# Kernel optimization log

Measured on AMD Instinct MI355X. Metric: run time of the kernel, lower is better.

The kernel has to match this reference:

```python
import jax, jax.numpy as jnp
import numpy as np
from jax import lax

EPS = 1e-5  # BatchNorm eps; eval-mode BN with running_mean=0, running_var=1


def _bn(v, g, b):
    return v * (g / jnp.sqrt(1.0 + EPS)) + b


def setup_inputs() -> dict:
    key = jax.random.key(0)
    ks = jax.random.split(key, 8)
    B, I, O, H, W, E, K, r = 16, 128, 128, 128, 128, 16, 3, 8
    Ir, Or = I // r, O // r
    f = jax.random.normal
    return {
        "x": f(ks[0], (B, I, H, W), jnp.float32),
        "experts": f(ks[1], (E, O, I, K, K), jnp.float32) * 0.05,
        "rw1": f(ks[2], (Ir, I), jnp.float32) * 0.05,
        "rbn1_g": jnp.ones((Ir,), jnp.float32),
        "rbn1_b": jnp.zeros((Ir,), jnp.float32),
        "rw2": f(ks[3], (I, Ir), jnp.float32) * 0.05,
        "rbn2_g": jnp.ones((I,), jnp.float32),
        "rbn2_b": jnp.zeros((I,), jnp.float32),
        "rw3": f(ks[4], (E, I), jnp.float32) * 0.05,
        "rb3": jnp.zeros((E,), jnp.float32),
        "ca_w1": f(ks[5], (Or, O), jnp.float32) * 0.05,
        "ca_bn1_g": jnp.ones((Or,), jnp.float32),
        "ca_bn1_b": jnp.zeros((Or,), jnp.float32),
        "ca_w2": f(ks[6], (O, Or), jnp.float32) * 0.05,
        "ca_bn2_g": jnp.ones((O,), jnp.float32),
        "ca_bn2_b": jnp.zeros((O,), jnp.float32),
        "sa_w": f(ks[7], (1, 2, 7, 7), jnp.float32) * 0.05,
        "sa_bn_g": jnp.ones((1,), jnp.float32),
        "sa_bn_b": jnp.zeros((1,), jnp.float32),
    }


def reference(x, experts, rw1, rbn1_g, rbn1_b, rw2, rbn2_g, rbn2_b, rw3, rb3,
              ca_w1, ca_bn1_g, ca_bn1_b, ca_w2, ca_bn2_g, ca_bn2_b,
              sa_w, sa_bn_g, sa_bn_b):
    B, I, H, W = x.shape
    E, O, _, K, _ = experts.shape
    # --- routing: avgpool -> 1x1 conv (matmul) -> BN -> ReLU -> 1x1 -> BN -> sigmoid -> 1x1 -> softmax
    p = jnp.mean(x, axis=(2, 3))                                  # [B, I]
    h = jax.nn.relu(_bn(p @ rw1.T, rbn1_g, rbn1_b))               # [B, I/r]
    g = jax.nn.sigmoid(_bn(h @ rw2.T, rbn2_g, rbn2_b))            # [B, I]
    rweights = jax.nn.softmax(g @ rw3.T + rb3, axis=1)            # [B, E]
    # --- expert-weighted kernel generation as a single GEMM
    w = jnp.einsum('be,eoihw->boihw', rweights, experts)          # [B, O, I, K, K]
    # --- per-sample conv via grouped conv (groups = B), stride=1, padding=1
    out = lax.conv_general_dilated(
        x.reshape(1, B * I, H, W),
        w.reshape(B * O, I, K, K),
        window_strides=(1, 1), padding=((1, 1), (1, 1)),
        dimension_numbers=('NCHW', 'OIHW', 'NCHW'),
        feature_group_count=B,
    ).reshape(B, O, H, W)
    # --- SE channel attention
    cp = jnp.mean(out, axis=(2, 3))                               # [B, O]
    ch = jax.nn.relu(_bn(cp @ ca_w1.T, ca_bn1_g, ca_bn1_b))
    cw = jax.nn.sigmoid(_bn(ch @ ca_w2.T, ca_bn2_g, ca_bn2_b))    # [B, O]
    out = out * cw[:, :, None, None]
    # --- CBAM spatial attention
    sp = jnp.concatenate([jnp.mean(out, axis=1, keepdims=True),
                          jnp.max(out, axis=1, keepdims=True)], axis=1)  # [B,2,H,W]
    sw = lax.conv_general_dilated(sp, sa_w, (1, 1), ((3, 3), (3, 3)),
                                  dimension_numbers=('NCHW', 'OIHW', 'NCHW'))
    sw = jax.nn.sigmoid(_bn(sw, sa_bn_g.reshape(1, 1, 1, 1), sa_bn_b.reshape(1, 1, 1, 1)))
    out = out * sw
    # --- residual (in_channels == out_channels -> Identity)
    return out + x
```

## Files before the change

kernel.cpp:

```cpp
#include <hip/hip_runtime.h>

typedef unsigned short ushort_t;
typedef __attribute__((ext_vector_type(4))) float float4_t;
typedef __attribute__((ext_vector_type(8))) short short8_t;
typedef __attribute__((ext_vector_type(8))) unsigned short ushort8_t;
typedef __attribute__((ext_vector_type(4))) unsigned short ushort4_t;

__device__ __forceinline__ ushort_t f2bf(float f) {
    unsigned u = __builtin_bit_cast(unsigned, f);
    u = (u + 0x7fffu + ((u >> 16) & 1u)) >> 16;
    return (ushort_t)u;
}
__device__ __forceinline__ ushort_t f2h(float f) {
    return __builtin_bit_cast(unsigned short, (_Float16)f);
}
__device__ __forceinline__ float h2f(ushort_t u) {
    return (float)__builtin_bit_cast(_Float16, u);
}

__device__ __forceinline__ void gld16(const void* g, void* l) {
    __builtin_amdgcn_global_load_lds(
        (const __attribute__((address_space(1))) unsigned int*)g,
        (__attribute__((address_space(3))) unsigned int*)l, 16, 0, 0);
}


__global__ __launch_bounds__(256) void init_kernel(float* __restrict__ p,
                                                   float* __restrict__ sp,
                                                   ushort_t* __restrict__ xn,
                                                   float* __restrict__ st,
                                                   unsigned* __restrict__ wcnt,
                                                   const float* __restrict__ x) {
    int blk = blockIdx.x;
    int tid = threadIdx.x;
    if (blk >= 6381) {
        int bi = blk - 6381;
        const float* xb = x + (long)bi * 16384;
        int half = tid >> 7, t = tid & 127;
        __shared__ float red[2][2][128];
        __shared__ float corn[4];
        float rv = half ? xb[16256 + t] : xb[t];
        float cv = half ? xb[t * 128 + 127] : xb[t * 128];
        red[0][half][t] = rv;
        red[1][half][t] = cv;
        if (tid == 0)   corn[0] = rv;
        if (tid == 127) corn[1] = rv;
        if (tid == 128) corn[2] = rv;
        if (tid == 255) corn[3] = rv;
        __syncthreads();
        int wave = tid >> 6, lane = tid & 63;
        int kind = wave >> 1, hf = wave & 1;
        float s = red[kind][hf][lane] + red[kind][hf][lane + 64];
        for (int msk = 1; msk < 64; msk <<= 1) s += __shfl_xor(s, msk, 64);
        if (lane == 0) st[bi * 8 + kind * 2 + hf] = s;
        if (tid < 4) st[bi * 8 + 4 + tid] = corn[tid];
        return;
    }
    int t = blk * 256 + tid;
    if (t < 2048) { p[t] = 0.f; if (t == 0) *wcnt = 0u; return; }
    t -= 2048;
    if (t < 574592) { sp[t] = 0.f; return; }
    t -= 574592;
    if (t < 1056768) {
        int b = t / 66048;
        int r = t % 66048;
        int pix = r >> 7, i = r & 127;
        int hp, wp;
        if (pix < 130)      { hp = 0;   wp = pix; }
        else if (pix < 260) { hp = 129; wp = pix - 130; }
        else { int q = pix - 260; hp = 1 + (q >> 1); wp = (q & 1) ? 129 : 0; }
        xn[((b * 130 + hp) * 130 + wp) * 128 + i] = 0;
    }
}

__global__ __launch_bounds__(256) void transpose_kernel(const float* __restrict__ x,
                                                        ushort_t* __restrict__ xn,
                                                        float* __restrict__ p) {
    __shared__ float tile[128][65];
    int blk = blockIdx.x;
    int wt = blk & 1, h = (blk >> 1) & 127, b = blk >> 8;
    int w0 = wt * 64;
    int tid = threadIdx.x;
    int wl = tid & 63, ig = tid >> 6;
    const float* src = x + ((long)(b * 128) * 128 + h) * 128 + w0 + wl;
    #pragma unroll
    for (int i = ig; i < 128; i += 4) tile[i][wl] = src[(long)i * 16384];
    __syncthreads();
    if (tid < 128) {
        float s = 0.f;
        #pragma unroll
        for (int w = 0; w < 64; ++w) s += tile[tid][w];
        atomicAdd(&p[b * 128 + tid], s * (1.0f / 16384.0f));
    }
    int l16 = tid & 15, wq = tid >> 4;
    #pragma unroll
    for (int pass = 0; pass < 4; ++pass) {
        int w = wq + pass * 16;
        ushort8_t v;
        #pragma unroll
        for (int j = 0; j < 8; ++j) v[j] = f2bf(tile[l16 * 8 + j][w]);
        *(ushort8_t*)&xn[((b * 130 + h + 1) * 130 + (w0 + w + 1)) * 128 + l16 * 8] = v;
    }
}

__global__ __launch_bounds__(256) void wgen_kernel(const float* __restrict__ experts,
        const float* __restrict__ p, const float* __restrict__ st,
        const float* __restrict__ rw1, const float* __restrict__ g1, const float* __restrict__ b1,
        const float* __restrict__ rw2, const float* __restrict__ g2, const float* __restrict__ b2,
        const float* __restrict__ rw3, const float* __restrict__ rb3,
        const float* __restrict__ cw1, const float* __restrict__ cg1, const float* __restrict__ cb1,
        const float* __restrict__ cw2, const float* __restrict__ cg2, const float* __restrict__ cb2,
        ushort_t* __restrict__ w2, float* __restrict__ cp, float* __restrict__ cw,
        unsigned* __restrict__ wcnt) {
    int o = blockIdx.x;
    int tid = threadIdx.x;
    int lane = tid & 63, wave = tid >> 6;
    __shared__ __align__(16) float ex[16 * 1152];
    __shared__ float sg[16][128];
    __shared__ float sh[16][16];
    __shared__ float sl[16][16];
    __shared__ float rwl[16][16];
    __shared__ float cpw[4][8];
    __shared__ int lastf;

    const float* ebase = experts + (long)o * 1152;
    #pragma unroll
    for (int j = 0; j < 4; ++j) {
        int e = wave * 4 + j;
        const char* src = (const char*)(ebase + (long)e * 147456) + lane * 16;
        char* dst = (char*)&ex[e * 1152];
        #pragma unroll
        for (int k = 0; k < 5; ++k) {
            if (k < 4 || lane < 32)
                gld16(src + k * 1024, dst + k * 1024);
        }
    }

    const float bns = rsqrtf(1.0f + 1e-5f);
    {   int b = tid >> 4, j = tid & 15;
        float s = 0.f;
        for (int i = 0; i < 128; ++i) s += p[b * 128 + i] * rw1[j * 128 + i];
        s = s * (g1[j] * bns) + b1[j];
        sh[b][j] = fmaxf(s, 0.f); }
    __syncthreads();
    for (int c = 0; c < 8; ++c) {
        int idx = tid + c * 256;
        int b = idx >> 7, j = idx & 127;
        float s = 0.f;
        for (int k = 0; k < 16; ++k) s += sh[b][k] * rw2[j * 16 + k];
        s = s * (g2[j] * bns) + b2[j];
        sg[b][j] = 1.0f / (1.0f + expf(-s));
    }
    __syncthreads();
    {   int b = tid >> 4, e = tid & 15;
        float s = rb3[e];
        for (int j = 0; j < 128; ++j) s += sg[b][j] * rw3[e * 128 + j];
        sl[b][e] = s; }
    __syncthreads();
    {   int b = tid >> 4, e = tid & 15;
        float m = -1e30f;
        for (int k = 0; k < 16; ++k) m = fmaxf(m, sl[b][k]);
        float num = expf(sl[b][e] - m), den = 0.f;
        for (int k = 0; k < 16; ++k) den += expf(sl[b][k] - m);
        rwl[b][e] = num / den; }
    asm volatile("s_waitcnt vmcnt(0)" ::: "memory");
    __syncthreads();

    int i = tid & 127, half = tid >> 7;
    float acc[8][9];
    #pragma unroll
    for (int b = 0; b < 8; ++b)
        #pragma unroll
        for (int d = 0; d < 9; ++d) acc[b][d] = 0.f;
    for (int e = 0; e < 16; ++e) {
        float v[9];
        #pragma unroll
        for (int d = 0; d < 9; ++d) v[d] = ex[e * 1152 + i * 9 + d];
        #pragma unroll
        for (int b = 0; b < 8; ++b) {
            float r = rwl[half * 8 + b][e];
            #pragma unroll
            for (int d = 0; d < 9; ++d) acc[b][d] += v[d] * r;
        }
    }
    float cps[8];
    #pragma unroll
    for (int bb2 = 0; bb2 < 8; ++bb2) {
        int b = half * 8 + bb2;
        const float* sb = st + ((b << 7) + i) * 8;
        float T = p[(b << 7) + i] * 16384.f;
        float r0 = sb[0], r127 = sb[1], c0 = sb[2], c127 = sb[3];
        float x00 = sb[4], x0127 = sb[5], x1270 = sb[6], x127127 = sb[7];
        float S0 = T - r127 - c127 + x127127;
        float S1 = T - r127;
        float S2 = T - r127 - c0 + x1270;
        float S3 = T - c127;
        float S4 = T;
        float S5 = T - c0;
        float S6 = T - r0 - c127 + x0127;
        float S7 = T - r0;
        float S8 = T - r0 - c0 + x00;
        cps[bb2] = acc[bb2][0] * S0 + acc[bb2][1] * S1 + acc[bb2][2] * S2 +
                   acc[bb2][3] * S3 + acc[bb2][4] * S4 + acc[bb2][5] * S5 +
                   acc[bb2][6] * S6 + acc[bb2][7] * S7 + acc[bb2][8] * S8;
    }
    #pragma unroll
    for (int bb2 = 0; bb2 < 8; ++bb2)
        for (int msk = 1; msk < 64; msk <<= 1) cps[bb2] += __shfl_xor(cps[bb2], msk, 64);
    if (lane == 0) {
        #pragma unroll
        for (int bb2 = 0; bb2 < 8; ++bb2) cpw[wave][bb2] = cps[bb2];
    }
    #pragma unroll
    for (int b = 0; b < 8; ++b)
        #pragma unroll
        for (int d = 0; d < 9; ++d)
            w2[(((half * 8 + b) * 9 + d) << 14) + (o << 7) + i] = f2bf(acc[b][d]);
    __syncthreads();
    if (tid < 16) {
        int hf = tid >> 3, idx = tid & 7;
        float v = cpw[hf * 2][idx] + cpw[hf * 2 + 1][idx];
        __hip_atomic_store(&cp[(tid << 7) + o], v, __ATOMIC_RELAXED,
                           __HIP_MEMORY_SCOPE_AGENT);
    }

    __threadfence();
    __syncthreads();
    if (tid == 0) lastf = (atomicAdd(wcnt, 1u) == 127u) ? 1 : 0;
    __syncthreads();
    if (!lastf) return;
    __threadfence();
    for (int c = 0; c < 8; ++c) {
        int idx = tid + c * 256;
        float v = __hip_atomic_load(&cp[idx], __ATOMIC_RELAXED, __HIP_MEMORY_SCOPE_AGENT);
        sg[idx >> 7][idx & 127] = v * (1.0f / 16384.0f);
    }
    __syncthreads();
    {   int b = tid >> 4, j = tid & 15;
        float s = 0.f;
        for (int oo = 0; oo < 128; ++oo) s += sg[b][oo] * cw1[j * 128 + oo];
        s = s * (cg1[j] * bns) + cb1[j];
        sh[b][j] = fmaxf(s, 0.f); }
    __syncthreads();
    for (int c = 0; c < 8; ++c) {
        int idx = tid + c * 256;
        int b = idx >> 7, oo = idx & 127;
        float s = 0.f;
        #pragma unroll
        for (int k = 0; k < 16; ++k) s += sh[b][k] * cw2[oo * 16 + k];
        s = s * (cg2[oo] * bns) + cb2[oo];
        cw[idx] = 1.0f / (1.0f + expf(-s));
    }
}

struct __align__(16) ConvSmem {
    union {
        struct { ushort_t X[16640]; ushort_t A[4][2][2048]; } t;
        float c[4224];
    };
};

__global__ __launch_bounds__(256, 2) void conv_kernel(const ushort_t* __restrict__ xn,
                                                      const ushort_t* __restrict__ w2,
                                                      const float* __restrict__ cw,
                                                      ushort_t* __restrict__ outi,
                                                      float* __restrict__ sp) {
    __shared__ ConvSmem sm;
    __shared__ float scw[128];
    __shared__ float cmb[2][128];
    int bh = (blockIdx.x & 7) * 256 + (blockIdx.x >> 3);
    int b = bh >> 7, h = bh & 127;
    int tid = threadIdx.x;
    int lane = tid & 63, wave = tid >> 6;
    int wm = wave >> 1, wn = wave & 1;
    int q = lane >> 4, nl = lane & 15;

    float4_t acc[4][4];
    #pragma unroll
    for (int mi = 0; mi < 4; ++mi)
        #pragma unroll
        for (int ni = 0; ni < 4; ++ni) acc[mi][ni] = (float4_t){0.f, 0.f, 0.f, 0.f};

    const ushort_t* xbase = xn + (b * 130 + h) * 16640;
    const ushort_t* abase = w2 + (long)b * 147456 + (wm * 64) * 128;

    auto stageX = [&](int dy) {
        const ushort_t* xrow = xbase + dy * 16640;
        #pragma unroll
        for (int seg = wave; seg < 33; seg += 4) {
            if (seg < 32 || lane < 32) {
                int lofs = seg * 512 + lane * 8;
                int pp = lofs >> 7;
                int jb = (lofs & 127) >> 3;
                gld16(xrow + (pp << 7) + ((jb ^ (pp & 15)) << 3), &sm.t.X[seg * 512]);
            }
        }
    };
    auto stageA = [&](int c) {
        int dy = c / 12, rem = c % 12, dx = rem >> 2, ic = rem & 3;
        const ushort_t* ab = abase + (dy * 3 + dx) * 16384 + ic * 32;
        ushort_t* dst = &sm.t.A[wave][c & 1][0];
        int ol = lane >> 2;
        int jsrc = (lane & 3) ^ ((ol >> 1) & 3);
        #pragma unroll
        for (int inst = 0; inst < 4; ++inst) {
            int ob = inst * 16;
            gld16(ab + (ob + ol) * 128 + (jsrc << 3), dst + ob * 32);
        }
    };

    short8_t afr[2][4], bfr[2][4];
    auto readFrag = [&](int cc) {
        int pb = cc & 1;
        int dx = (cc % 12) >> 2, ic = cc & 3;
        const ushort_t* ap = &sm.t.A[wave][cc & 1][0];
        #pragma unroll
        for (int mi = 0; mi < 4; ++mi) {
            int ol = mi * 16 + nl;
            afr[pb][mi] = *(const short8_t*)&ap[(ol << 5) + ((q ^ ((ol >> 1) & 3)) << 3)];
        }
        #pragma unroll
        for (int ni = 0; ni < 4; ++ni) {
            int pp = wn * 64 + ni * 16 + nl + dx;
            int J = ic * 4 + q;
            bfr[pb][ni] = *(const short8_t*)&sm.t.X[(pp << 7) + ((J ^ (pp & 15)) << 3)];
        }
    };
    auto domfmaH = [&](int pb, int m0) {
        __builtin_amdgcn_s_setprio(1);
        #pragma unroll
        for (int mi = m0; mi < m0 + 2; ++mi)
            #pragma unroll
            for (int ni = 0; ni < 4; ++ni)
                acc[mi][ni] = __builtin_amdgcn_mfma_f32_16x16x32_bf16(
                    afr[pb][mi], bfr[pb][ni], acc[mi][ni], 0, 0, 0);
        __builtin_amdgcn_s_setprio(0);
    };

    stageX(0);
    stageA(0); stageA(1);
    asm volatile("s_waitcnt vmcnt(0)" ::: "memory");
    __builtin_amdgcn_s_barrier();
    readFrag(0);

    #pragma unroll
    for (int c = 0; c < 36; ++c) {
        if (c + 2 < 36) stageA(c + 2);
        domfmaH(c & 1, 0);
        const bool bnd = (c == 11 || c == 23);
        if (!bnd && c + 1 < 36) {
            if (c == 34) asm volatile("s_waitcnt vmcnt(0)" ::: "memory");
            else         asm volatile("s_waitcnt vmcnt(4)" ::: "memory");
            readFrag(c + 1);
        }
        domfmaH(c & 1, 2);
        if (bnd) {
            __builtin_amdgcn_s_barrier();
            stageX(c == 11 ? 1 : 2);
            asm volatile("s_waitcnt vmcnt(0)" ::: "memory");
            __builtin_amdgcn_s_barrier();
            readFrag(c + 1);
        }
    }

    ushort_t* outb = outi + (((long)(b << 7)) << 14) + (h << 7);
    if (tid < 128) scw[tid] = cw[(b << 7) + tid];
    int wpx = tid & 127, g = tid >> 7;
    float wsum = 0.f, wmax = -1e30f;
    #pragma unroll
    for (int os = 0; os < 4; ++os) {
        __syncthreads();
        if (wm == (os >> 1)) {
            #pragma unroll
            for (int mi2 = 0; mi2 < 2; ++mi2) {
                int mi = (os & 1) * 2 + mi2;
                #pragma unroll
                for (int ni = 0; ni < 4; ++ni) {
                    float4_t v = acc[mi][ni];
                    int orow = mi2 * 16 + q * 4;
                    int w = wn * 64 + ni * 16 + nl;
                    #pragma unroll
                    for (int rr = 0; rr < 4; ++rr) sm.c[(orow + rr) * 132 + w] = v[rr];
                }
            }
        }
        __syncthreads();
        int row = tid >> 4, j = tid & 15;
        #pragma unroll
        for (int pass = 0; pass < 2; ++pass) {
            int r2 = pass * 16 + row;
            ushort8_t v;
            #pragma unroll
            for (int k = 0; k < 8; ++k) v[k] = f2h(sm.c[r2 * 132 + j * 8 + k]);
            *(ushort8_t*)&outb[((long)(os * 32 + r2) << 14) + j * 8] = v;
        }
        #pragma unroll
        for (int r = 0; r < 16; ++r) {
            int orow = g * 16 + r;
            float v = sm.c[orow * 132 + wpx] * scw[os * 32 + orow];
            wsum += v;
            wmax = fmaxf(wmax, v);
        }
    }
    if (g == 1) { cmb[0][wpx] = wsum; cmb[1][wpx] = wmax; }
    __syncthreads();
    if (g == 0) {
        wsum += cmb[0][wpx];
        wmax = fmaxf(wmax, cmb[1][wpx]);
        float* d = sp + b * 2 * 17956;
        d[(h + 3) * 134 + (wpx + 3)] = wsum * (1.0f / 128.0f);
        d[17956 + (h + 3) * 134 + (wpx + 3)] = wmax;
    }
}

__global__ __launch_bounds__(256) void sattn_kernel(const float* __restrict__ sp,
        const float* __restrict__ k98, const float* __restrict__ g, const float* __restrict__ bb,
        const float* __restrict__ cw, const float* __restrict__ x,
        const ushort_t* __restrict__ outi, float* __restrict__ out) {
    int b = blockIdx.x >> 7, h = blockIdx.x & 127;
    int tid = threadIdx.x;
    __shared__ float ls[2][7][134];
    __shared__ float lk[98];
    __shared__ float sws[128];
    __shared__ float scw[128];
    const float* sb = sp + b * 2 * 17956;
    for (int idx = tid; idx < 2 * 7 * 134; idx += 256) {
        int c = idx / 938, rr = idx % 938;
        int ky = rr / 134, wp = rr % 134;
        ls[c][ky][wp] = sb[c * 17956 + (h + ky) * 134 + wp];
    }
    if (tid < 98) lk[tid] = k98[tid];
    if (tid >= 128) scw[tid - 128] = cw[(b << 7) + (tid - 128)];
    __syncthreads();
    if (tid < 128) {
        float s = 0.f;
        #pragma unroll
        for (int c = 0; c < 2; ++c)
            #pragma unroll
            for (int ky = 0; ky < 7; ++ky)
                #pragma unroll
                for (int kx = 0; kx < 7; ++kx)
                    s += ls[c][ky][tid + kx] * lk[c * 49 + ky * 7 + kx];
        s = s * (g[0] * rsqrtf(1.0f + 1e-5f)) + bb[0];
        sws[tid] = 1.0f / (1.0f + expf(-s));
    }
    __syncthreads();
    int w4 = tid & 31, og = tid >> 5;
    long base = (((long)b << 21) + (h << 7)) + (w4 << 2);
    float4_t sv = *(const float4_t*)&sws[w4 << 2];
    #pragma unroll
    for (int o = og; o < 128; o += 8) {
        long idx = base + ((long)o << 14);
        ushort4_t hv = *(const ushort4_t*)&outi[idx];
        float4_t ov = (float4_t){h2f(hv[0]), h2f(hv[1]), h2f(hv[2]), h2f(hv[3])};
        float4_t xv = *(const float4_t*)&x[idx];
        float4_t r = ov * scw[o] * sv + xv;
        *(float4_t*)&out[idx] = r;
    }
}

extern "C" void kernel_launch(void* const* d_in, const int* in_sizes, int n_in,
                              void* d_out, int out_size, void* d_ws, size_t ws_size,
                              hipStream_t stream) {
    const float* x       = (const float*)d_in[0];
    const float* experts = (const float*)d_in[1];
    const float* rw1     = (const float*)d_in[2];
    const float* rbn1_g  = (const float*)d_in[3];
    const float* rbn1_b  = (const float*)d_in[4];
    const float* rw2     = (const float*)d_in[5];
    const float* rbn2_g  = (const float*)d_in[6];
    const float* rbn2_b  = (const float*)d_in[7];
    const float* rw3     = (const float*)d_in[8];
    const float* rb3     = (const float*)d_in[9];
    const float* ca_w1   = (const float*)d_in[10];
    const float* ca_bn1g = (const float*)d_in[11];
    const float* ca_bn1b = (const float*)d_in[12];
    const float* ca_w2   = (const float*)d_in[13];
    const float* ca_bn2g = (const float*)d_in[14];
    const float* ca_bn2b = (const float*)d_in[15];
    const float* sa_w    = (const float*)d_in[16];
    const float* sa_g    = (const float*)d_in[17];
    const float* sa_b    = (const float*)d_in[18];
    float* out = (float*)d_out;
    char* ws = (char*)d_ws;

    ushort_t* xn   = (ushort_t*)(ws);
    ushort_t* w2   = (ushort_t*)(ws + 69222400);
    float*    p    = (float*)(ws + 73940992);
    float*    cp   = (float*)(ws + 73949184);
    unsigned* wcnt = (unsigned*)(ws + 73957376);
    float*    cw   = (float*)(ws + 73958400);
    float*    sp   = (float*)(ws + 73966592);
    ushort_t* outi = (ushort_t*)(ws + 76264960);
    float*    st   = (float*)(ws + 143373824);

    hipLaunchKernelGGL(init_kernel, dim3(8429), dim3(256), 0, stream,
                       p, sp, xn, st, wcnt, x);
    hipLaunchKernelGGL(transpose_kernel, dim3(4096), dim3(256), 0, stream, x, xn, p);
    hipLaunchKernelGGL(wgen_kernel, dim3(128), dim3(256), 0, stream,
                       experts, p, st, rw1, rbn1_g, rbn1_b, rw2, rbn2_g, rbn2_b, rw3, rb3,
                       ca_w1, ca_bn1g, ca_bn1b, ca_w2, ca_bn2g, ca_bn2b,
                       w2, cp, cw, wcnt);
    hipLaunchKernelGGL(conv_kernel, dim3(2048), dim3(256), 0, stream, xn, w2, cw, outi, sp);
    hipLaunchKernelGGL(sattn_kernel, dim3(2048), dim3(256), 0, stream,
                       sp, sa_w, sa_g, sa_b, cw, x, outi, out);
}
```

Measured before the change: 472.9 us.

## Parallelize weight generation over batch pairs and read residual from bf16 copy

The weight-generation kernel now launches one block per (output channel, batch pair), 1024 blocks instead of 128. Each block computes routing only for its two samples, which raises parallelism but reloads the expert slice eight times. The spatial-attention epilogue now reads the residual from the padded bf16 channels-last copy of x, staged and transposed through LDS, instead of the fp32 input. This halves the residual read traffic but adds bf16 rounding error to the output.

Result: slower. 533.3 us (+12.8%).

```diff
diff --git a/kernel.cpp b/kernel.cpp
--- a/kernel.cpp
+++ b/kernel.cpp
@@ -5,11 +5,15 @@
 typedef __attribute__((ext_vector_type(8))) short short8_t;
 typedef __attribute__((ext_vector_type(8))) unsigned short ushort8_t;
 typedef __attribute__((ext_vector_type(4))) unsigned short ushort4_t;
+typedef __attribute__((ext_vector_type(4))) unsigned int uint4_t;
 
 __device__ __forceinline__ ushort_t f2bf(float f) {
     unsigned u = __builtin_bit_cast(unsigned, f);
     u = (u + 0x7fffu + ((u >> 16) & 1u)) >> 16;
     return (ushort_t)u;
+}
+__device__ __forceinline__ float bf2f(ushort_t u) {
+    return __builtin_bit_cast(float, (unsigned)u << 16);
 }
 __device__ __forceinline__ ushort_t f2h(float f) {
     return __builtin_bit_cast(unsigned short, (_Float16)f);
@@ -112,15 +116,16 @@
         const float* __restrict__ cw2, const float* __restrict__ cg2, const float* __restrict__ cb2,
         ushort_t* __restrict__ w2, float* __restrict__ cp, float* __restrict__ cw,
         unsigned* __restrict__ wcnt) {
-    int o = blockIdx.x;
+    int o = blockIdx.x & 127, bg = blockIdx.x >> 7;
+    int b0 = bg * 2;
     int tid = threadIdx.x;
     int lane = tid & 63, wave = tid >> 6;
     __shared__ __align__(16) float ex[16 * 1152];
-    __shared__ float sg[16][128];
-    __shared__ float sh[16][16];
-    __shared__ float sl[16][16];
-    __shared__ float rwl[16][16];
-    __shared__ float cpw[4][8];
+    __shared__ float sh2[2][16];
+    __shared__ float sg2[2][128];
+    __shared__ float sl2[2][16];
+    __shared__ float rwl2[2][16];
+    __shared__ float cpw[4];
     __shared__ int lastf;
 
     const float* ebase = experts + (long)o * 1152;
@@ -137,56 +142,53 @@
     }
 
     const float bns = rsqrtf(1.0f + 1e-5f);
-    {   int b = tid >> 4, j = tid & 15;
+    if (tid < 32) {
+        int bh = tid >> 4, j = tid & 15;
         float s = 0.f;
-        for (int i = 0; i < 128; ++i) s += p[b * 128 + i] * rw1[j * 128 + i];
+        for (int i = 0; i < 128; ++i) s += p[(b0 + bh) * 128 + i] * rw1[j * 128 + i];
         s = s * (g1[j] * bns) + b1[j];
-        sh[b][j] = fmaxf(s, 0.f); }
-    __syncthreads();
-    for (int c = 0; c < 8; ++c) {
-        int idx = tid + c * 256;
-        int b = idx >> 7, j = idx & 127;
+        sh2[bh][j] = fmaxf(s, 0.f);
+    }
+    __syncthreads();
+    {   int bh = tid >> 7, j = tid & 127;
         float s = 0.f;
-        for (int k = 0; k < 16; ++k) s += sh[b][k] * rw2[j * 16 + k];
+        #pragma unroll
+        for (int k = 0; k < 16; ++k) s += sh2[bh][k] * rw2[j * 16 + k];
         s = s * (g2[j] * bns) + b2[j];
-        sg[b][j] = 1.0f / (1.0f + expf(-s));
-    }
-    __syncthreads();
-    {   int b = tid >> 4, e = tid & 15;
+        sg2[bh][j] = 1.0f / (1.0f + expf(-s)); }
+    __syncthreads();
+    if (tid < 32) {
+        int bh = tid >> 4, e = tid & 15;
         float s = rb3[e];
-        for (int j = 0; j < 128; ++j) s += sg[b][j] * rw3[e * 128 + j];
-        sl[b][e] = s; }
-    __syncthreads();
-    {   int b = tid >> 4, e = tid & 15;
+        for (int j = 0; j < 128; ++j) s += sg2[bh][j] * rw3[e * 128 + j];
+        sl2[bh][e] = s;
+    }
+    __syncthreads();
+    if (tid < 32) {
+        int bh = tid >> 4, e = tid & 15;
         float m = -1e30f;
-        for (int k = 0; k < 16; ++k) m = fmaxf(m, sl[b][k]);
-        float num = expf(sl[b][e] - m), den = 0.f;
-        for (int k = 0; k < 16; ++k) den += expf(sl[b][k] - m);
-        rwl[b][e] = num / den; }
+        #pragma unroll
+        for (int k = 0; k < 16; ++k) m = fmaxf(m, sl2[bh][k]);
+        float num = expf(sl2[bh][e] - m), den = 0.f;
+        #pragma unroll
+        for (int k = 0; k < 16; ++k) den += expf(sl2[bh][k] - m);
+        rwl2[bh][e] = num / den;
+    }
     asm volatile("s_waitcnt vmcnt(0)" ::: "memory");
     __syncthreads();
 
     int i = tid & 127, half = tid >> 7;
-    float acc[8][9];
-    #pragma unroll
-    for (int b = 0; b < 8; ++b)
-        #pragma unroll
-        for (int d = 0; d < 9; ++d) acc[b][d] = 0.f;
+    int b = b0 + half;
+    float acc[9];
+    #pragma unroll
+    for (int d = 0; d < 9; ++d) acc[d] = 0.f;
     for (int e = 0; e < 16; ++e) {
-        float v[9];
-        #pragma unroll
-        for (int d = 0; d < 9; ++d) v[d] = ex[e * 1152 + i * 9 + d];
-        #pragma unroll
-        for (int b = 0; b < 8; ++b) {
-            float r = rwl[half * 8 + b][e];
-            #pragma unroll
-            for (int d = 0; d < 9; ++d) acc[b][d] += v[d] * r;
-        }
-    }
-    float cps[8];
-    #pragma unroll
-    for (int bb2 = 0; bb2 < 8; ++bb2) {
-        int b = half * 8 + bb2;
+        float r = rwl2[half][e];
+        #pragma unroll
+        for (int d = 0; d < 9; ++d) acc[d] += ex[e * 1152 + i * 9 + d] * r;
+    }
+    float cps;
+    {
         const float* sb = st + ((b << 7) + i) * 8;
         float T = p[(b << 7) + i] * 16384.f;
         float r0 = sb[0], r127 = sb[1], c0 = sb[2], c127 = sb[3];
@@ -200,54 +202,49 @@
         float S6 = T - r0 - c127 + x0127;
         float S7 = T - r0;
         float S8 = T - r0 - c0 + x00;
-        cps[bb2] = acc[bb2][0] * S0 + acc[bb2][1] * S1 + acc[bb2][2] * S2 +
-                   acc[bb2][3] * S3 + acc[bb2][4] * S4 + acc[bb2][5] * S5 +
-                   acc[bb2][6] * S6 + acc[bb2][7] * S7 + acc[bb2][8] * S8;
-    }
-    #pragma unroll
-    for (int bb2 = 0; bb2 < 8; ++bb2)
-        for (int msk = 1; msk < 64; msk <<= 1) cps[bb2] += __shfl_xor(cps[bb2], msk, 64);
-    if (lane == 0) {
-        #pragma unroll
-        for (int bb2 = 0; bb2 < 8; ++bb2) cpw[wave][bb2] = cps[bb2];
-    }
-    #pragma unroll
-    for (int b = 0; b < 8; ++b)
-        #pragma unroll
-        for (int d = 0; d < 9; ++d)
-            w2[(((half * 8 + b) * 9 + d) << 14) + (o << 7) + i] = f2bf(acc[b][d]);
-    __syncthreads();
-    if (tid < 16) {
-        int hf = tid >> 3, idx = tid & 7;
-        float v = cpw[hf * 2][idx] + cpw[hf * 2 + 1][idx];
-        __hip_atomic_store(&cp[(tid << 7) + o], v, __ATOMIC_RELAXED,
+        cps = acc[0] * S0 + acc[1] * S1 + acc[2] * S2 +
+              acc[3] * S3 + acc[4] * S4 + acc[5] * S5 +
+              acc[6] * S6 + acc[7] * S7 + acc[8] * S8;
+    }
+    for (int msk = 1; msk < 64; msk <<= 1) cps += __shfl_xor(cps, msk, 64);
+    if (lane == 0) cpw[wave] = cps;
+    #pragma unroll
+    for (int d = 0; d < 9; ++d)
+        w2[(((b * 9 + d) << 14) + (o << 7)) + i] = f2bf(acc[d]);
+    __syncthreads();
+    if (tid == 0)
+        __hip_atomic_store(&cp[(b0 << 7) + o], cpw[0] + cpw[1], __ATOMIC_RELAXED,
                            __HIP_MEMORY_SCOPE_AGENT);
-    }
+    if (tid == 128)
+        __hip_atomic_store(&cp[((b0 + 1) << 7) + o], cpw[2] + cpw[3], __ATOMIC_RELAXED,
+                           __HIP_MEMORY_SCOPE_AGENT);
 
     __threadfence();
     __syncthreads();
-    if (tid == 0) lastf = (atomicAdd(wcnt, 1u) == 127u) ? 1 : 0;
+    if (tid == 0) lastf = (atomicAdd(wcnt, 1u) == 1023u) ? 1 : 0;
     __syncthreads();
     if (!lastf) return;
     __threadfence();
+    float* sc  = ex;
+    float* shs = ex + 2048;
     for (int c = 0; c < 8; ++c) {
         int idx = tid + c * 256;
         float v = __hip_atomic_load(&cp[idx], __ATOMIC_RELAXED, __HIP_MEMORY_SCOPE_AGENT);
-        sg[idx >> 7][idx & 127] = v * (1.0f / 16384.0f);
-    }
-    __syncthreads();
-    {   int b = tid >> 4, j = tid & 15;
+        sc[idx] = v * (1.0f / 16384.0f);
+    }
+    __syncthreads();
+    {   int bb = tid >> 4, j = tid & 15;
         float s = 0.f;
-        for (int oo = 0; oo < 128; ++oo) s += sg[b][oo] * cw1[j * 128 + oo];
+        for (int oo = 0; oo < 128; ++oo) s += sc[bb * 128 + oo] * cw1[j * 128 + oo];
         s = s * (cg1[j] * bns) + cb1[j];
-        sh[b][j] = fmaxf(s, 0.f); }
+        shs[bb * 16 + j] = fmaxf(s, 0.f); }
     __syncthreads();
     for (int c = 0; c < 8; ++c) {
         int idx = tid + c * 256;
-        int b = idx >> 7, oo = idx & 127;
+        int bb = idx >> 7, oo = idx & 127;
         float s = 0.f;
         #pragma unroll
-        for (int k = 0; k < 16; ++k) s += sh[b][k] * cw2[oo * 16 + k];
+        for (int k = 0; k < 16; ++k) s += shs[bb * 16 + k] * cw2[oo * 16 + k];
         s = s * (cg2[oo] * bns) + cb2[oo];
         cw[idx] = 1.0f / (1.0f + expf(-s));
     }
@@ -415,7 +412,7 @@
 
 __global__ __launch_bounds__(256) void sattn_kernel(const float* __restrict__ sp,
         const float* __restrict__ k98, const float* __restrict__ g, const float* __restrict__ bb,
-        const float* __restrict__ cw, const float* __restrict__ x,
+        const float* __restrict__ cw, const ushort_t* __restrict__ xn,
         const ushort_t* __restrict__ outi, float* __restrict__ out) {
     int b = blockIdx.x >> 7, h = blockIdx.x & 127;
     int tid = threadIdx.x;
@@ -423,7 +420,19 @@
     __shared__ float lk[98];
     __shared__ float sws[128];
     __shared__ float scw[128];
+    __shared__ unsigned lx[128][67];
     const float* sb = sp + b * 2 * 17956;
+    const ushort_t* xr = xn + ((long)(b * 130 + h + 1) * 130 + 1) * 128;
+    #pragma unroll
+    for (int it = 0; it < 8; ++it) {
+        int idx = tid + it * 256;
+        int w = idx >> 4, c = idx & 15;
+        uint4_t v = *(const uint4_t*)&xr[w * 128 + c * 8];
+        lx[w][c * 4 + 0] = v[0];
+        lx[w][c * 4 + 1] = v[1];
+        lx[w][c * 4 + 2] = v[2];
+        lx[w][c * 4 + 3] = v[3];
+    }
     for (int idx = tid; idx < 2 * 7 * 134; idx += 256) {
         int c = idx / 938, rr = idx % 938;
         int ky = rr / 134, wp = rr % 134;
@@ -453,7 +462,13 @@
         long idx = base + ((long)o << 14);
         ushort4_t hv = *(const ushort4_t*)&outi[idx];
         float4_t ov = (float4_t){h2f(hv[0]), h2f(hv[1]), h2f(hv[2]), h2f(hv[3])};
-        float4_t xv = *(const float4_t*)&x[idx];
+        float4_t xv;
+        #pragma unroll
+        for (int k = 0; k < 4; ++k) {
+            unsigned u = lx[w4 * 4 + k][o >> 1];
+            ushort_t xb = (o & 1) ? (ushort_t)(u >> 16) : (ushort_t)(u & 0xffffu);
+            xv[k] = bf2f(xb);
+        }
         float4_t r = ov * scw[o] * sv + xv;
         *(float4_t*)&out[idx] = r;
     }
@@ -497,11 +512,11 @@
     hipLaunchKernelGGL(init_kernel, dim3(8429), dim3(256), 0, stream,
                        p, sp, xn, st, wcnt, x);
     hipLaunchKernelGGL(transpose_kernel, dim3(4096), dim3(256), 0, stream, x, xn, p);
-    hipLaunchKernelGGL(wgen_kernel, dim3(128), dim3(256), 0, stream,
+    hipLaunchKernelGGL(wgen_kernel, dim3(1024), dim3(256), 0, stream,
                        experts, p, st, rw1, rbn1_g, rbn1_b, rw2, rbn2_g, rbn2_b, rw3, rb3,
                        ca_w1, ca_bn1g, ca_bn1b, ca_w2, ca_bn2g, ca_bn2b,
                        w2, cp, cw, wcnt);
     hipLaunchKernelGGL(conv_kernel, dim3(2048), dim3(256), 0, stream, xn, w2, cw, outi, sp);
     hipLaunchKernelGGL(sattn_kernel, dim3(2048), dim3(256), 0, stream,
-                       sp, sa_w, sa_g, sa_b, cw, x, outi, out);
-}
+                       sp, sa_w, sa_g, sa_b, cw, xn, outi, out);
+}
```
